# Optimization experiments

Measured on AMD Instinct MI355X. Metric: run time of the kernel, lower is better.

Reference implementation:

```python
import jax, jax.numpy as jnp
import numpy as np

B, N, H, F, DIN, NC = 4, 1024, 8, 256, 256, 10  # batch graphs, nodes, heads, feat/head, input dim, classes


def setup_inputs() -> dict:
    key = jax.random.key(0)
    ks = jax.random.split(key, 12)
    def rn(k, shape, s=0.05):
        return jax.random.normal(k, shape, jnp.float32) * s
    return dict(
        features=rn(ks[0], (B, N, DIN), 1.0),
        eigvects=rn(ks[1], (B, N, DIN), 1.0),  # unused by forward, mirrors original signature
        attn_mask=jnp.zeros((B, N, N), jnp.float32),  # additive mask: 0 = edge, -inf = no edge
        W1=rn(ks[2], (DIN, H * F)), a_src1=rn(ks[3], (H, F)), a_tgt1=rn(ks[4], (H, F)),
        skip1=rn(ks[5], (DIN, H * F)), b1=jnp.zeros((H * F,), jnp.float32),
        W2=rn(ks[6], (H * F, H * F)), a_src2=rn(ks[7], (H, F)), a_tgt2=rn(ks[8], (H, F)),
        skip2=rn(ks[9], (H * F, H * F)), b2=jnp.zeros((F,), jnp.float32),
        Wc=rn(ks[10], (F, NC)), bc=jnp.zeros((NC,), jnp.float32),
    )


def _gat_layer(x, mask, W, a_s, a_t, skipW, b, concat):
    # GAT IMP2: dense all-pairs scores + additive connectivity mask. Dropout is eval-mode identity.
    Bb, Nn, _ = x.shape
    Hh, Ff = a_s.shape
    p = (x @ W).reshape(Bb, Nn, Hh, Ff)                      # projected node features (B,N,H,F)
    s_src = jnp.einsum('bnhf,hf->bnh', p, a_s)
    s_tgt = jnp.einsum('bnhf,hf->bnh', p, a_t)
    # score[b,i,j,h] = leaky(src_i + tgt_j) + mask[b,i,j]
    scores = jax.nn.leaky_relu(s_src[:, :, None, :] + s_tgt[:, None, :, :], 0.2) + mask[..., None]
    attn = jax.nn.softmax(scores, axis=2)                    # softmax over neighbors j
    out = jnp.einsum('bijh,bjhf->bihf', attn, p)
    out = out + (x @ skipW).reshape(Bb, Nn, Hh, Ff)          # skip connection (projected)
    out = out.reshape(Bb, Nn, Hh * Ff) if concat else out.mean(axis=2)
    out = out + b
    return jax.nn.elu(out) if concat else out


def reference(features, eigvects, attn_mask, W1, a_src1, a_tgt1, skip1, b1,
              W2, a_src2, a_tgt2, skip2, b2, Wc, bc):
    x = _gat_layer(features, attn_mask, W1, a_src1, a_tgt1, skip1, b1, True)   # (B,N,H*F), ELU
    x = _gat_layer(x, attn_mask, W2, a_src2, a_tgt2, skip2, b2, False)         # (B,N,F), heads averaged
    g = x.mean(axis=1)                                                         # mean pool over nodes
    return g @ Wc + bc                                                         # (B, n_classes)
```

## Files before the change

kernel.cpp:

```cpp
#include <hip/hip_runtime.h>
#include <hip/hip_bf16.h>
#include <stdint.h>
#include <stddef.h>

typedef __hip_bfloat16 bf16;
typedef __attribute__((ext_vector_type(8))) short bhalf8;
typedef __attribute__((ext_vector_type(4))) short short4v;
typedef __attribute__((ext_vector_type(4))) float floatx4;

static __device__ __forceinline__ float b2f(bf16 v) { return __bfloat162float(v); }
static __device__ __forceinline__ bf16  f2b(float v) { return __float2bfloat16(v); }
static __device__ __forceinline__ short f2s(float v) {
    union { bf16 b; short s; } u; u.b = __float2bfloat16(v); return u.s;
}
static __device__ __forceinline__ float s2f(short v) {
    union { short s; bf16 b; } u; u.s = v; return b2f(u.b);
}

static __device__ __forceinline__ float loadf(const void* p, size_t i, int f32) {
    return f32 ? ((const float*)p)[i] : b2f(((const bf16*)p)[i]);
}

static __device__ __forceinline__ void gl_lds16(const void* g, void* l) {
    __builtin_amdgcn_global_load_lds(
        (const __attribute__((address_space(1))) void*)g,
        (__attribute__((address_space(3))) void*)l, 16, 0, 0);
}

static __device__ __forceinline__ void load_mask4b(const bf16* m, size_t idx,
                                                   float* mv) {
    short4v v = *(const short4v*)(m + idx);
    #pragma unroll
    for (int t = 0; t < 4; t++) mv[t] = s2f(v[t]);
}

__global__ __launch_bounds__(256) void prep_k(const void* __restrict__ feat,
                                              bf16* __restrict__ featc,
                                              const void* __restrict__ mask,
                                              bf16* __restrict__ maskb,
                                              float* __restrict__ zbase, int nzero,
                                              const void* __restrict__ W1,
                                              bf16* __restrict__ W1t,
                                              const void* __restrict__ skip1,
                                              bf16* __restrict__ S1t,
                                              const void* __restrict__ W2,
                                              const void* __restrict__ a_src1,
                                              const void* __restrict__ a_tgt1,
                                              const void* __restrict__ a_src2,
                                              const void* __restrict__ a_tgt2,
                                              bf16* __restrict__ Wa1b,
                                              bf16* __restrict__ Wa2b,
                                              int* __restrict__ flagp)
{
    __shared__ int sflag;
    __shared__ bf16 tile[32][33];
    const int tid = threadIdx.x;

    if (tid < 64) {
        const unsigned short* s = (const unsigned short*)W1;
        int bad = 0;
        #pragma unroll
        for (int i = 0; i < 4; i++) {
            int e = (s[tid * 4 + i] >> 7) & 0xFF;
            if (e > 0x85 || (e != 0 && e < 0x60)) bad++;
        }
        bad += __shfl_xor(bad, 1, 64);
        bad += __shfl_xor(bad, 2, 64);
        bad += __shfl_xor(bad, 4, 64);
        bad += __shfl_xor(bad, 8, 64);
        bad += __shfl_xor(bad, 16, 64);
        bad += __shfl_xor(bad, 32, 64);
        if (tid == 0) sflag = (bad > 16) ? 1 : 0;
    }
    __syncthreads();
    const int f32 = sflag;

    int id = blockIdx.x;
    if (id == 0 && tid == 0) *flagp = f32;

    if (id < 4096) {
        const int i = id * 256 + tid;
        featc[i] = f32 ? f2b(((const float*)feat)[i]) : ((const bf16*)feat)[i];
        return;
    }
    id -= 4096;
    if (id < 4096) {
        const size_t i = (size_t)id * 1024 + tid * 4;
        if (f32) {
            float4 v = *(const float4*)((const float*)mask + i);
            short4v o;
            o[0] = f2s(v.x); o[1] = f2s(v.y); o[2] = f2s(v.z); o[3] = f2s(v.w);
            *(short4v*)(maskb + i) = o;
        } else {
            *(short4v*)(maskb + i) = *(const short4v*)((const bf16*)mask + i);
        }
        return;
    }
    id -= 4096;
    if (id < 480) {
        const int i = id * 256 + tid;
        if (i < nzero) zbase[i] = 0.f;
        return;
    }
    id -= 480;
    if (id < 1024) {
        const void* in = (id < 512) ? W1 : skip1;
        bf16* out = (id < 512) ? W1t : S1t;
        const int t = id & 511;
        const int bx = t & 63, byy = t >> 6;
        const int tx = tid & 31, ty = tid >> 5;
        const int c0 = bx * 32, r0 = byy * 32;
        #pragma unroll
        for (int yy = ty; yy < 32; yy += 8)
            tile[yy][tx] = f2b(loadf(in, (size_t)(r0 + yy) * 2048 + c0 + tx, f32));
        __syncthreads();
        #pragma unroll
        for (int yy = ty; yy < 32; yy += 8)
            out[(size_t)(c0 + yy) * 256 + r0 + tx] = tile[tx][yy];
        return;
    }
    id -= 1024;
    if (id < 512) {
        const int wave = tid >> 6, lane = tid & 63;
        const int base = id * 64;
        const int hh = base >> 11, h = hh & 7;
        const void* a = (hh < 8) ? a_src2 : a_tgt2;
        float av[4];
        #pragma unroll
        for (int i = 0; i < 4; i++) av[i] = loadf(a, h * 256 + lane * 4 + i, f32);
        #pragma unroll 4
        for (int o = 0; o < 16; o++) {
            const int idx = base + wave * 16 + o;
            const int k = idx & 2047;
            float acc = 0.f;
            #pragma unroll
            for (int i = 0; i < 4; i++)
                acc = fmaf(loadf(W2, (size_t)k * 2048 + h * 256 + lane * 4 + i, f32),
                           av[i], acc);
            #pragma unroll
            for (int off2 = 32; off2; off2 >>= 1) acc += __shfl_down(acc, off2, 64);
            if (lane == 0) Wa2b[idx] = f2b(acc);
        }
        return;
    }
    id -= 512;
    {
        const int wave = tid >> 6, lane = tid & 63;
        const int base = id * 64;
        const int hh = base >> 8, h = hh & 7;
        const void* a = (hh < 8) ? a_src1 : a_tgt1;
        float av[4];
        #pragma unroll
        for (int i = 0; i < 4; i++) av[i] = loadf(a, h * 256 + lane * 4 + i, f32);
        #pragma unroll 4
        for (int o = 0; o < 16; o++) {
            const int idx = base + wave * 16 + o;
            const int k = idx & 255;
            float acc = 0.f;
            #pragma unroll
            for (int i = 0; i < 4; i++)
                acc = fmaf(loadf(W1, (size_t)k * 2048 + h * 256 + lane * 4 + i, f32),
                           av[i], acc);
            #pragma unroll
            for (int off2 = 32; off2; off2 >>= 1) acc += __shfl_down(acc, off2, 64);
            if (lane == 0) Wa1b[idx] = f2b(acc);
        }
    }
}

__global__ __launch_bounds__(256) void gemm_dual(const bf16* __restrict__ featc,
                                                 const bf16* __restrict__ W1t,
                                                 const bf16* __restrict__ S1t,
                                                 bf16* __restrict__ pT,
                                                 bf16* __restrict__ sk1)
{
    __shared__ __align__(16) short sA[128][32];
    __shared__ __align__(16) short sB[128][32];
    const int tid = threadIdx.x;
    const int z = blockIdx.z;
    const bf16* A  = z ? featc : W1t;
    const bf16* Bt = z ? S1t   : featc;
    const int mbase = (z ? blockIdx.x : blockIdx.y) * 128;
    const int nbase = (z ? blockIdx.y : blockIdx.x) * 128;
    const int wave = tid >> 6, lane = tid & 63;
    const int wm = wave >> 1, wn = wave & 1;
    const int lrow = lane & 15, quad = lane >> 4;

    floatx4 acc[4][4];
    #pragma unroll
    for (int i = 0; i < 4; i++)
        #pragma unroll
        for (int j = 0; j < 4; j++)
            acc[i][j] = (floatx4){0.f, 0.f, 0.f, 0.f};

    const int srow = wave * 32 + (lane >> 2);
    const int scol = (lane & 3) * 8;
    const bf16* gA0 = A  + (size_t)(mbase + srow) * 256 + scol;
    const bf16* gA1 = gA0 + (size_t)16 * 256;
    const bf16* gB0 = Bt + (size_t)(nbase + srow) * 256 + scol;
    const bf16* gB1 = gB0 + (size_t)16 * 256;
    char* lA0 = (char*)&sA[0][0] + wave * 2048 + lane * 16;
    char* lA1 = lA0 + 1024;
    char* lB0 = (char*)&sB[0][0] + wave * 2048 + lane * 16;
    char* lB1 = lB0 + 1024;

    for (int k0 = 0; k0 < 256; k0 += 32) {
        __syncthreads();
        gl_lds16(gA0 + k0, lA0);
        gl_lds16(gA1 + k0, lA1);
        gl_lds16(gB0 + k0, lB0);
        gl_lds16(gB1 + k0, lB1);
        __syncthreads();
        bhalf8 af[4], bfr[4];
        #pragma unroll
        for (int t = 0; t < 4; t++) af[t]  = *(const bhalf8*)&sA[wm * 64 + t * 16 + lrow][quad * 8];
        #pragma unroll
        for (int t = 0; t < 4; t++) bfr[t] = *(const bhalf8*)&sB[wn * 64 + t * 16 + lrow][quad * 8];
        #pragma unroll
        for (int tm = 0; tm < 4; tm++)
            #pragma unroll
            for (int tn = 0; tn < 4; tn++)
                acc[tm][tn] = __builtin_amdgcn_mfma_f32_16x16x32_bf16(af[tm], bfr[tn], acc[tm][tn], 0, 0, 0);
    }

    #pragma unroll
    for (int tm = 0; tm < 4; tm++) {
        #pragma unroll
        for (int tn = 0; tn < 4; tn++) {
            const int col = nbase + wn * 64 + tn * 16 + lrow;
            #pragma unroll
            for (int r = 0; r < 4; r++) {
                const int row = mbase + wm * 64 + tm * 16 + quad * 4 + r;
                if (z) {
                    sk1[(size_t)row * 2048 + col] = f2b(acc[tm][tn][r]);
                } else {
                    const size_t idx = ((size_t)((col >> 10) * 8 + (row >> 8)) << 18)
                                     + (size_t)(row & 255) * 1024 + (col & 1023);
                    pT[idx] = f2b(acc[tm][tn][r]);
                }
            }
        }
    }
}

template <int K>
__global__ __launch_bounds__(256) void score_k(const bf16* __restrict__ X,
                                               const bf16* __restrict__ Wab,
                                               float* __restrict__ ss,
                                               float* __restrict__ st)
{
    constexpr int VPL = K / 64;
    const int wave = threadIdx.x >> 6, lane = threadIdx.x & 63;
    const int n = blockIdx.x * 4 + wave;
    const int b = n >> 10, nn = n & 1023;

    const bf16* xr = X + (size_t)n * K + lane * VPL;
    float xv[VPL];
    if (VPL == 4) {
        short4v v = *(const short4v*)xr;
        #pragma unroll
        for (int t = 0; t < 4; t++) xv[t] = s2f(v[t]);
    } else {
        #pragma unroll
        for (int c = 0; c < VPL / 8; c++) {
            bhalf8 v = *(const bhalf8*)(xr + c * 8);
            #pragma unroll
            for (int t = 0; t < 8; t++) xv[c * 8 + t] = s2f(v[t]);
        }
    }

    #pragma unroll
    for (int hh = 0; hh < 16; hh++) {
        const bf16* wr = Wab + (size_t)hh * K + lane * VPL;
        float acc = 0.f;
        if (VPL == 4) {
            short4v v = *(const short4v*)wr;
            #pragma unroll
            for (int t = 0; t < 4; t++) acc = fmaf(xv[t], s2f(v[t]), acc);
        } else {
            #pragma unroll
            for (int c = 0; c < VPL / 8; c++) {
                bhalf8 v = *(const bhalf8*)(wr + c * 8);
                #pragma unroll
                for (int t = 0; t < 8; t++) acc = fmaf(xv[c * 8 + t], s2f(v[t]), acc);
            }
        }
        #pragma unroll
        for (int off = 32; off; off >>= 1) acc += __shfl_down(acc, off, 64);
        if (lane == 0) {
            const int h = hh & 7;
            if (hh < 8) ss[(b * 8 + h) * 1024 + nn] = acc;
            else        st[(b * 8 + h) * 1024 + nn] = acc;
        }
    }
}

__global__ __launch_bounds__(256) void attn_fused(const float* __restrict__ s_src_t,
                                                  const float* __restrict__ s_tgt_t,
                                                  const bf16* __restrict__ maskb,
                                                  const bf16* __restrict__ pT,
                                                  const bf16* __restrict__ sk,
                                                  const void* __restrict__ bias,
                                                  bf16* __restrict__ x2,
                                                  const int* __restrict__ flag)
{
    __shared__ __align__(16) short sA[2][32][32];
    __shared__ short sStgt[1024];
    __shared__ float sInvl[32];

    const int tid = threadIdx.x;
    const int d = blockIdx.x;
    const int L = (d & 7) * 128 + (d >> 3);
    const int by = L & 31, bh = L >> 5;
    const int b = bh >> 3, h = bh & 7;
    const int f32 = *flag;
    const int wave = tid >> 6, lane = tid & 63;
    const int lrow = lane & 15, quad = lane >> 4;

    #pragma unroll
    for (int q = 0; q < 4; q++)
        sStgt[q * 256 + tid] = f2s(s_tgt_t[bh * 1024 + q * 256 + tid]);

    const int row  = tid >> 3;
    const int col0 = (tid & 7) * 4;
    const float ssr = s_src_t[bh * 1024 + by * 32 + row];
    const size_t mrow0 = ((size_t)(b * 1024 + by * 32 + row)) << 10;

    const bf16* gBf = pT + ((size_t)bh << 18)
                    + (size_t)(wave * 64 + lrow) * 1024 + quad * 8;

    floatx4 acc[2][4];
    #pragma unroll
    for (int i = 0; i < 2; i++)
        #pragma unroll
        for (int j = 0; j < 4; j++)
            acc[i][j] = (floatx4){0.f, 0.f, 0.f, 0.f};

    float lacc = 0.f;

    auto genA = [&](int k0, int buf, const float* mv) {
        const short* sp = &sStgt[k0 + col0];
        short4v ev;
        #pragma unroll
        for (int t = 0; t < 4; t++) {
            float x = ssr + s2f(sp[t]);
            x = fmaxf(x, 0.2f * x);
            float e = __expf(x + mv[t]);
            lacc += e;
            ev[t] = f2s(e);
        }
        *(short4v*)&sA[buf][row][col0] = ev;
    };

    bhalf8 bcur[4], bnxt[4];
    #pragma unroll
    for (int nt = 0; nt < 4; nt++)
        bcur[nt] = *(const bhalf8*)(gBf + (size_t)(nt * 16) * 1024);

    float mv[4];
    load_mask4b(maskb, mrow0 + col0, mv);
    genA(0, 0, mv);
    load_mask4b(maskb, mrow0 + 32 + col0, mv);

    int cur = 0;
    for (int k0 = 0; k0 < 1024; k0 += 32, cur ^= 1) {
        __syncthreads();
        if (k0 + 32 < 1024) {
            #pragma unroll
            for (int nt = 0; nt < 4; nt++)
                bnxt[nt] = *(const bhalf8*)(gBf + (size_t)(nt * 16) * 1024 + k0 + 32);
            genA(k0 + 32, cur ^ 1, mv);
            if (k0 + 64 < 1024)
                load_mask4b(maskb, mrow0 + k0 + 64 + col0, mv);
        }
        bhalf8 af[2];
        #pragma unroll
        for (int mt = 0; mt < 2; mt++)
            af[mt] = *(const bhalf8*)&sA[cur][mt * 16 + lrow][quad * 8];
        #pragma unroll
        for (int mt = 0; mt < 2; mt++)
            #pragma unroll
            for (int nt = 0; nt < 4; nt++)
                acc[mt][nt] = __builtin_amdgcn_mfma_f32_16x16x32_bf16(af[mt], bcur[nt], acc[mt][nt], 0, 0, 0);
        if (k0 + 32 < 1024) {
            #pragma unroll
            for (int nt = 0; nt < 4; nt++) bcur[nt] = bnxt[nt];
        }
    }

    lacc += __shfl_xor(lacc, 1, 64);
    lacc += __shfl_xor(lacc, 2, 64);
    lacc += __shfl_xor(lacc, 4, 64);
    if ((tid & 7) == 0) sInvl[row] = 1.0f / lacc;
    __syncthreads();

    #pragma unroll
    for (int mt = 0; mt < 2; mt++) {
        #pragma unroll
        for (int r = 0; r < 4; r++) {
            const int rl = mt * 16 + quad * 4 + r;
            const int rg = by * 32 + rl;
            const float il = sInvl[rl];
            #pragma unroll
            for (int nt = 0; nt < 4; nt++) {
                const int col = wave * 64 + nt * 16 + lrow;
                const int hf = h * 256 + col;
                const size_t idx = ((size_t)(b * 1024 + rg)) * 2048 + hf;
                float v = acc[mt][nt][r] * il + b2f(sk[idx]) + loadf(bias, hf, f32);
                v = (v > 0.f) ? v : expm1f(v);
                x2[idx] = f2b(v);
            }
        }
    }
}

__global__ __launch_bounds__(256) void colsoft_k(const float* __restrict__ s_src_t,
                                                 const float* __restrict__ s_tgt_t,
                                                 const bf16* __restrict__ maskb,
                                                 float* __restrict__ c)
{
    __shared__ float sS[64];
    __shared__ float sIl[64];
    const int bh = blockIdx.x, iz = blockIdx.y, b = bh >> 3;
    const int tid = threadIdx.x;
    const int i0 = iz * 64;
    if (tid < 64) sS[tid] = s_src_t[bh * 1024 + i0 + tid];
    __syncthreads();

    {
        const int row = tid >> 2, c4 = tid & 3;
        const float ssr = sS[row];
        const size_t mrow = ((size_t)(b * 1024 + i0 + row)) << 10;
        float l = 0.f;
        #pragma unroll 4
        for (int q = 0; q < 64; q++) {
            const int j = c4 * 256 + q * 4;
            float mv[4];
            load_mask4b(maskb, mrow + j, mv);
            float4 s4 = *(const float4*)(s_tgt_t + bh * 1024 + j);
            float sv[4] = {s4.x, s4.y, s4.z, s4.w};
            #pragma unroll
            for (int t = 0; t < 4; t++) {
                float x = ssr + sv[t];
                x = fmaxf(x, 0.2f * x);
                l += __expf(x + mv[t]);
            }
        }
        l += __shfl_xor(l, 1, 64);
        l += __shfl_xor(l, 2, 64);
        if ((tid & 3) == 0) sIl[row] = 1.0f / l;
    }
    __syncthreads();

    const int j0 = tid * 4;
    float4 s4 = *(const float4*)(s_tgt_t + bh * 1024 + j0);
    float sv[4] = {s4.x, s4.y, s4.z, s4.w};
    float a[4] = {0.f, 0.f, 0.f, 0.f};
    #pragma unroll 4
    for (int r = 0; r < 64; r++) {
        const float sr = sS[r], il = sIl[r];
        float mv[4];
        load_mask4b(maskb, (((size_t)(b * 1024 + i0 + r)) << 10) + j0, mv);
        #pragma unroll
        for (int t = 0; t < 4; t++) {
            float x = sr + sv[t];
            x = fmaxf(x, 0.2f * x);
            a[t] = fmaf(il, __expf(x + mv[t]), a[t]);
        }
    }
    #pragma unroll
    for (int t = 0; t < 4; t++)
        atomicAdd(&c[bh * 1024 + j0 + t], a[t]);
}

__global__ __launch_bounds__(256) void yx_k(const bf16* __restrict__ x2,
                                            const float* __restrict__ c,
                                            float* __restrict__ y,
                                            float* __restrict__ xbar)
{
    __shared__ float sC[8][32];
    const int b = blockIdx.x, kt = blockIdx.y, jc = blockIdx.z;
    const int t = threadIdx.x;
    const int k = kt * 512 + t * 2;
    const int j0 = jc * 32;
    {
        const int h = t >> 5, jj = t & 31;
        sC[h][jj] = c[(b * 8 + h) * 1024 + j0 + jj];
    }
    __syncthreads();
    float acc0[8] = {0.f, 0.f, 0.f, 0.f, 0.f, 0.f, 0.f, 0.f};
    float acc1[8] = {0.f, 0.f, 0.f, 0.f, 0.f, 0.f, 0.f, 0.f};
    float ax0 = 0.f, ax1 = 0.f;
    #pragma unroll 4
    for (int jj = 0; jj < 32; jj++) {
        const unsigned int v =
            *(const unsigned int*)&x2[((size_t)(b * 1024 + j0 + jj)) * 2048 + k];
        const float x0 = s2f((short)(v & 0xffff));
        const float x1 = s2f((short)(v >> 16));
        ax0 += x0; ax1 += x1;
        #pragma unroll
        for (int h = 0; h < 8; h++) {
            acc0[h] = fmaf(sC[h][jj], x0, acc0[h]);
            acc1[h] = fmaf(sC[h][jj], x1, acc1[h]);
        }
    }
    #pragma unroll
    for (int h = 0; h < 8; h++) {
        atomicAdd(&y[(b * 8 + h) * 2048 + k], acc0[h]);
        atomicAdd(&y[(b * 8 + h) * 2048 + k + 1], acc1[h]);
    }
    atomicAdd(&xbar[b * 2048 + k], ax0);
    atomicAdd(&xbar[b * 2048 + k + 1], ax1);
}

__global__ __launch_bounds__(256) void gs_k(const void* __restrict__ W2,
                                            const void* __restrict__ skip2,
                                            const float* __restrict__ y,
                                            const float* __restrict__ xbar,
                                            float* __restrict__ gA,
                                            float* __restrict__ gS,
                                            const int* __restrict__ flagp)
{
    __shared__ float sY[64];
    const int f32 = *flagp;
    int id = blockIdx.x;
    if (id < 1024) {
        const int bh = id & 31, kc = id >> 5;
        const int h = bh & 7, f = threadIdx.x;
        const int k0 = kc * 64;
        if (threadIdx.x < 64) sY[threadIdx.x] = y[bh * 2048 + k0 + threadIdx.x];
        __syncthreads();
        float acc = 0.f;
        #pragma unroll 4
        for (int kk = 0; kk < 64; kk++)
            acc = fmaf(sY[kk], loadf(W2, (size_t)(k0 + kk) * 2048 + h * 256 + f, f32), acc);
        atomicAdd(&gA[bh * 256 + f], acc);
    } else {
        const int idx = id - 1024;
        const int b = idx & 3, hft = (idx >> 2) & 7, kc = idx >> 5;
        const int hf = hft * 256 + threadIdx.x;
        const int k0 = kc * 64;
        if (threadIdx.x < 64) sY[threadIdx.x] = xbar[b * 2048 + k0 + threadIdx.x];
        __syncthreads();
        float acc = 0.f;
        #pragma unroll 4
        for (int kk = 0; kk < 64; kk++)
            acc = fmaf(sY[kk], loadf(skip2, (size_t)(k0 + kk) * 2048 + hf, f32), acc);
        atomicAdd(&gS[b * 2048 + hf], acc);
    }
}

__global__ __launch_bounds__(256) void classify2_k(const float* __restrict__ gA,
                                                   const float* __restrict__ gS,
                                                   const void* __restrict__ b2,
                                                   const void* __restrict__ Wc,
                                                   const void* __restrict__ bc,
                                                   void* __restrict__ out,
                                                   const int* __restrict__ flag)
{
    __shared__ float gv[256];
    const int f32 = *flag;
    const int b = blockIdx.x, f = threadIdx.x;
    float s = 0.f;
    #pragma unroll
    for (int h = 0; h < 8; h++)
        s += gA[(b * 8 + h) * 256 + f] + gS[b * 2048 + h * 256 + f];
    gv[f] = s * (1.0f / 8192.0f) + loadf(b2, f, f32);
    __syncthreads();
    if (f < 10) {
        float acc = loadf(bc, f, f32);
        for (int k = 0; k < 256; k++)
            acc = fmaf(gv[k], loadf(Wc, k * 10 + f, f32), acc);
        if (f32) ((float*)out)[b * 10 + f] = acc;
        else     ((bf16*)out)[b * 10 + f] = f2b(acc);
    }
}

extern "C" void kernel_launch(void* const* d_in, const int* in_sizes, int n_in,
                              void* d_out, int out_size, void* d_ws, size_t ws_size,
                              hipStream_t stream)
{
    (void)in_sizes; (void)n_in; (void)out_size; (void)ws_size;
    const void* feat   = d_in[0];
    const void* mask   = d_in[2];
    const void* W1     = d_in[3];
    const void* a_src1 = d_in[4];
    const void* a_tgt1 = d_in[5];
    const void* skip1  = d_in[6];
    const void* b1     = d_in[7];
    const void* W2     = d_in[8];
    const void* a_src2 = d_in[9];
    const void* a_tgt2 = d_in[10];
    const void* skip2  = d_in[11];
    const void* b2v    = d_in[12];
    const void* Wc     = d_in[13];
    const void* bc     = d_in[14];

    char* ws = (char*)d_ws;
    size_t off = 0;
    auto alloc = [&](size_t bytes) -> void* {
        void* p = ws + off;
        off += (bytes + 255) & ~(size_t)255;
        return p;
    };
    int*   flag  = (int*)alloc(256);
    bf16*  featc = (bf16*)alloc(4096ull * 256 * 2);
    bf16*  maskb = (bf16*)alloc(4ull * 1024 * 1024 * 2);
    bf16*  W1t   = (bf16*)alloc(2048ull * 256 * 2);
    bf16*  S1t   = (bf16*)alloc(2048ull * 256 * 2);
    bf16*  sk1   = (bf16*)alloc(4096ull * 2048 * 2);
    bf16*  x2    = (bf16*)alloc(4096ull * 2048 * 2);
    bf16*  pT    = (bf16*)alloc(4096ull * 2048 * 2);
    float* ss    = (float*)alloc(32ull * 1024 * 4);
    float* st    = (float*)alloc(32ull * 1024 * 4);
    bf16*  Wa1b  = (bf16*)alloc(16ull * 256 * 2);
    bf16*  Wa2b  = (bf16*)alloc(16ull * 2048 * 2);
    float* cbuf = (float*)alloc(32ull * 1024 * 4);
    float* gA   = (float*)alloc(32ull * 256 * 4);
    float* gS   = (float*)alloc(4ull * 2048 * 4);
    float* xbar = (float*)alloc(4ull * 2048 * 4);
    float* y    = (float*)alloc(32ull * 2048 * 4);
    const int nzero = 32768 + 3 * 8192 + 65536;

    prep_k<<<10272, 256, 0, stream>>>(feat, featc, mask, maskb, cbuf, nzero,
                                      W1, W1t, skip1, S1t, W2,
                                      a_src1, a_tgt1, a_src2, a_tgt2,
                                      Wa1b, Wa2b, flag);
    gemm_dual<<<dim3(32, 16, 2), 256, 0, stream>>>(featc, W1t, S1t, pT, sk1);
    score_k<256><<<1024, 256, 0, stream>>>(featc, Wa1b, ss, st);
    attn_fused<<<1024, 256, 0, stream>>>(ss, st, maskb, pT, sk1, b1, x2, flag);
    score_k<2048><<<1024, 256, 0, stream>>>(x2, Wa2b, ss, st);
    colsoft_k<<<dim3(32, 16), 256, 0, stream>>>(ss, st, maskb, cbuf);
    yx_k<<<dim3(4, 4, 32), 256, 0, stream>>>(x2, cbuf, y, xbar);
    gs_k<<<2048, 256, 0, stream>>>(W2, skip2, y, xbar, gA, gS, flag);
    classify2_k<<<4, 256, 0, stream>>>(gA, gS, b2v, Wc, bc, d_out, flag);
}
```

Before: 374.3 us.

## Retile attention kernel to 64x128 tiles with LDS-staged B via async loads

Each block of the fused attention kernel now covers 64 query rows and half of the 256 feature columns (split by fh), instead of 32 rows and all columns. The B operand (pT) is staged into a double-buffered LDS tile with global_load_lds rather than loaded straight into registers, and the mask is read as 8-wide vectors. The aim is to raise MFMA work per exp computation and to overlap B transfers with compute. In exchange, the softmax exponentials are computed twice, once per feature half. The old XCD-aware block remapping is also dropped, so the host launch grid must match the new block indexing.

```diff
diff --git a/kernel.cpp b/kernel.cpp
--- a/kernel.cpp
+++ b/kernel.cpp
@@ -304,14 +304,14 @@
                                                   bf16* __restrict__ x2,
                                                   const int* __restrict__ flag)
 {
-    __shared__ __align__(16) short sA[2][32][32];
+    __shared__ __align__(16) short sA[2][64][32];
+    __shared__ __align__(16) short sB[2][128][32];
     __shared__ short sStgt[1024];
-    __shared__ float sInvl[32];
+    __shared__ float sInvl[64];
 
     const int tid = threadIdx.x;
     const int d = blockIdx.x;
-    const int L = (d & 7) * 128 + (d >> 3);
-    const int by = L & 31, bh = L >> 5;
+    const int by = d & 15, fh = (d >> 4) & 1, bh = d >> 5;
     const int b = bh >> 3, h = bh & 7;
     const int f32 = *flag;
     const int wave = tid >> 6, lane = tid & 63;
@@ -321,89 +321,92 @@
     for (int q = 0; q < 4; q++)
         sStgt[q * 256 + tid] = f2s(s_tgt_t[bh * 1024 + q * 256 + tid]);
 
-    const int row  = tid >> 3;
-    const int col0 = (tid & 7) * 4;
-    const float ssr = s_src_t[bh * 1024 + by * 32 + row];
-    const size_t mrow0 = ((size_t)(b * 1024 + by * 32 + row)) << 10;
-
-    const bf16* gBf = pT + ((size_t)bh << 18)
-                    + (size_t)(wave * 64 + lrow) * 1024 + quad * 8;
-
-    floatx4 acc[2][4];
-    #pragma unroll
-    for (int i = 0; i < 2; i++)
-        #pragma unroll
-        for (int j = 0; j < 4; j++)
+    const int row  = tid >> 2;
+    const int col0 = (tid & 3) * 8;
+    const float ssr = s_src_t[bh * 1024 + by * 64 + row];
+    const size_t mrow0 = ((size_t)(b * 1024 + by * 64 + row)) << 10;
+
+    const bf16* gB = pT + ((size_t)bh << 18)
+                   + (size_t)(fh * 128 + wave * 32 + (lane >> 2)) * 1024
+                   + (lane & 3) * 8;
+
+    floatx4 acc[4][2];
+    #pragma unroll
+    for (int i = 0; i < 4; i++)
+        #pragma unroll
+        for (int j = 0; j < 2; j++)
             acc[i][j] = (floatx4){0.f, 0.f, 0.f, 0.f};
 
     float lacc = 0.f;
 
-    auto genA = [&](int k0, int buf, const float* mv) {
+    auto stageB = [&](int k0, int buf) {
+        char* l = (char*)&sB[buf][0][0] + wave * 2048 + lane * 16;
+        #pragma unroll
+        for (int c = 0; c < 2; c++)
+            gl_lds16(gB + (size_t)(c * 16) * 1024 + k0, l + c * 1024);
+    };
+    auto genA = [&](int k0, int buf, bhalf8 m8) {
         const short* sp = &sStgt[k0 + col0];
-        short4v ev;
-        #pragma unroll
-        for (int t = 0; t < 4; t++) {
+        bhalf8 ev;
+        #pragma unroll
+        for (int t = 0; t < 8; t++) {
             float x = ssr + s2f(sp[t]);
             x = fmaxf(x, 0.2f * x);
-            float e = __expf(x + mv[t]);
+            float e = __expf(x + s2f(m8[t]));
             lacc += e;
             ev[t] = f2s(e);
         }
-        *(short4v*)&sA[buf][row][col0] = ev;
+        *(bhalf8*)&sA[buf][row][col0] = ev;
     };
-
-    bhalf8 bcur[4], bnxt[4];
-    #pragma unroll
-    for (int nt = 0; nt < 4; nt++)
-        bcur[nt] = *(const bhalf8*)(gBf + (size_t)(nt * 16) * 1024);
-
-    float mv[4];
-    load_mask4b(maskb, mrow0 + col0, mv);
-    genA(0, 0, mv);
-    load_mask4b(maskb, mrow0 + 32 + col0, mv);
+    auto loadmask = [&](int k0) -> bhalf8 {
+        return *(const bhalf8*)(maskb + mrow0 + k0 + col0);
+    };
+
+    stageB(0, 0);
+    bhalf8 mcur = loadmask(0);
+    __syncthreads();
+    genA(0, 0, mcur);
+    bhalf8 mnxt = loadmask(32);
 
     int cur = 0;
     for (int k0 = 0; k0 < 1024; k0 += 32, cur ^= 1) {
         __syncthreads();
         if (k0 + 32 < 1024) {
-            #pragma unroll
-            for (int nt = 0; nt < 4; nt++)
-                bnxt[nt] = *(const bhalf8*)(gBf + (size_t)(nt * 16) * 1024 + k0 + 32);
-            genA(k0 + 32, cur ^ 1, mv);
+            const int nxt = cur ^ 1;
+            stageB(k0 + 32, nxt);
+            genA(k0 + 32, nxt, mnxt);
             if (k0 + 64 < 1024)
-                load_mask4b(maskb, mrow0 + k0 + 64 + col0, mv);
-        }
-        bhalf8 af[2];
-        #pragma unroll
-        for (int mt = 0; mt < 2; mt++)
+                mnxt = loadmask(k0 + 64);
+        }
+        bhalf8 af[4], bfr[2];
+        #pragma unroll
+        for (int mt = 0; mt < 4; mt++)
             af[mt] = *(const bhalf8*)&sA[cur][mt * 16 + lrow][quad * 8];
         #pragma unroll
-        for (int mt = 0; mt < 2; mt++)
-            #pragma unroll
-            for (int nt = 0; nt < 4; nt++)
-                acc[mt][nt] = __builtin_amdgcn_mfma_f32_16x16x32_bf16(af[mt], bcur[nt], acc[mt][nt], 0, 0, 0);
-        if (k0 + 32 < 1024) {
-            #pragma unroll
-            for (int nt = 0; nt < 4; nt++) bcur[nt] = bnxt[nt];
-        }
+        for (int nt = 0; nt < 2; nt++)
+            bfr[nt] = *(const bhalf8*)&sB[cur][wave * 32 + nt * 16 + lrow][quad * 8];
+        #pragma unroll
+        for (int mt = 0; mt < 4; mt++)
+            #pragma unroll
+            for (int nt = 0; nt < 2; nt++)
+                acc[mt][nt] = __builtin_amdgcn_mfma_f32_16x16x32_bf16(af[mt], bfr[nt], acc[mt][nt], 0, 0, 0);
     }
 
     lacc += __shfl_xor(lacc, 1, 64);
     lacc += __shfl_xor(lacc, 2, 64);
-    lacc += __shfl_xor(lacc, 4, 64);
-    if ((tid & 7) == 0) sInvl[row] = 1.0f / lacc;
+    if ((tid & 3) == 0) sInvl[row] = 1.0f / lacc;
     __syncthreads();
 
     #pragma unroll
-    for (int mt = 0; mt < 2; mt++) {
+    for (int mt = 0; mt < 4; mt++) {
         #pragma unroll
         for (int r = 0; r < 4; r++) {
             const int rl = mt * 16 + quad * 4 + r;
-            const int rg = by * 32 + rl;
+            const int rg = by * 64 + rl;
             const float il = sInvl[rl];
             #pragma unroll
-            for (int nt = 0; nt < 4; nt++) {
-                const int col = wave * 64 + nt * 16 + lrow;
+            for (int nt = 0; nt < 2; nt++) {
+                const int col = fh * 128 + wave * 32 + nt * 16 + lrow;
                 const int hf = h * 256 + col;
                 const size_t idx = ((size_t)(b * 1024 + rg)) * 2048 + hf;
                 float v = acc[mt][nt][r] * il + b2f(sk[idx]) + loadf(bias, hf, f32);
```

After: 352.2 us. 1.06x faster.
